# Performance work log

Measured on AMD Instinct MI355X. Metric: run time of the kernel, lower is better.

The kernel has to match this reference:

```python
import jax, jax.numpy as jnp
import numpy as np


def _relative_position_index(wd, wh, ww):
    coords = np.stack(np.meshgrid(np.arange(wd), np.arange(wh), np.arange(ww), indexing='ij'))
    flat = coords.reshape(3, -1)                      # (3, N)
    rel = flat[:, :, None] - flat[:, None, :]         # (3, N, N)
    rel = rel.transpose(1, 2, 0).astype(np.int64)     # (N, N, 3)
    rel[..., 0] += wd - 1
    rel[..., 1] += wh - 1
    rel[..., 2] += ww - 1
    rel[..., 0] *= (2 * wh - 1) * (2 * ww - 1)
    rel[..., 1] *= (2 * ww - 1)
    return rel.sum(-1)                                 # (N, N)


def setup_inputs() -> dict:
    key = jax.random.key(0)
    k0, k1, k2, k3 = jax.random.split(key, 4)
    B, D, H, W = 4, 16, 56, 56
    wd, wh, ww = 8, 7, 7
    C, nH = 128, 4
    N = wd * wh * ww                                   # 392
    nW = (D // wd) * (H // wh) * (W // ww)             # 128
    B_ = B * nW                                        # 512
    table_sz = (2 * wd - 1) * (2 * wh - 1) * (2 * ww - 1)  # 2535
    x = jax.random.normal(k0, (B_, N, C), jnp.float32)
    mask = jnp.zeros((nW, N, N), jnp.float32)          # 0/-inf additive mask; zeros = no shift
    qkv_w = jax.random.normal(k1, (3 * C, C), jnp.float32) * 0.02
    proj_w = jax.random.normal(k2, (C, C), jnp.float32) * 0.02
    proj_b = jnp.zeros((C,), jnp.float32)
    bias_table = jax.random.normal(k3, (table_sz, nH), jnp.float32) * 0.02
    rel_index = jnp.asarray(_relative_position_index(wd, wh, ww), jnp.int32)
    return {"x": x, "mask": mask, "qkv_w": qkv_w, "proj_w": proj_w,
            "proj_b": proj_b, "bias_table": bias_table, "rel_index": rel_index}


def reference(x, mask, qkv_w, proj_w, proj_b, bias_table, rel_index):
    B_, N, C = x.shape
    nH = bias_table.shape[1]
    hd = C // nH
    scale = hd ** -0.5
    # qkv projection (no bias, qkv_bias=False)
    qkv = (x @ qkv_w.T).reshape(B_, N, 3, nH, hd).transpose(2, 0, 3, 1, 4)  # (3,B_,H,N,hd)
    q, k, v = qkv[0] * scale, qkv[1], qkv[2]
    attn = jnp.einsum('bhnd,bhmd->bhnm', q, k)                              # (B_,H,N,N)
    bias = bias_table[rel_index.reshape(-1)].reshape(N, N, nH).transpose(2, 0, 1)
    attn = attn + bias[None]
    nW = mask.shape[0]
    attn = attn.reshape(B_ // nW, nW, nH, N, N) + mask[None, :, None]
    attn = jax.nn.softmax(attn.reshape(B_, nH, N, N), axis=-1)
    out = jnp.einsum('bhnm,bhmd->bhnd', attn, v)                            # (B_,H,N,hd)
    out = out.transpose(0, 2, 1, 3).reshape(B_, N, C)
    return out @ proj_w.T + proj_b
```

## Files before the change

### kernel.cpp

```cpp
#include <hip/hip_runtime.h>

typedef unsigned short u16;
typedef unsigned int   u32;

#define NTOK   392
#define NN2    153664
#define LOG2E  1.44269504088896340736f
#define QSCL   (0.17677669529663687f * 1.44269504088896340736f)
#define BTK    416
#define BTH    (416L*416L)

typedef __attribute__((ext_vector_type(8))) __bf16 bf16x8;
typedef __attribute__((ext_vector_type(4))) float  f32x4;
#define MFMA16(a,b,c) __builtin_amdgcn_mfma_f32_16x16x32_bf16((a),(b),(c),0,0,0)

__device__ __forceinline__ float bf2f(u16 u){
    union { u32 i; float f; } v; v.i = ((u32)u) << 16; return v.f;
}
__device__ __forceinline__ u16 f2bf(float x){
    union { float f; u32 i; } v; v.f = x;
    u32 r = (v.i + 0x7FFFu + ((v.i >> 16) & 1u)) >> 16;
    return (u16)r;
}
__device__ __forceinline__ u16 bfbits(float x){
    union { __bf16 b; u16 u; } v; v.b = (__bf16)x; return v.u;
}
__device__ __forceinline__ u32 pk2(float a, float b){
    return (u32)bfbits(a) | ((u32)bfbits(b) << 16);
}
__device__ __forceinline__ float ldf(const void* p, int isb, long i){
    if (isb) return bf2f(((const u16*)p)[i]);
    else     return ((const float*)p)[i];
}
__device__ __forceinline__ void stf(void* p, int isb, long i, float v){
    if (isb) ((u16*)p)[i] = f2bf(v);
    else     ((float*)p)[i] = v;
}

__device__ __forceinline__ void ld8s(const void* p, int isb, long i0,
                                     bf16x8* h, bf16x8* l){
    union { u16 u[8]; bf16x8 v; } H, L;
    if (isb){
        const uint2* q = (const uint2*)((const u16*)p + i0);
        uint2 a = q[0], b = q[1];
        H.u[0]=(u16)a.x; H.u[1]=(u16)(a.x>>16); H.u[2]=(u16)a.y; H.u[3]=(u16)(a.y>>16);
        H.u[4]=(u16)b.x; H.u[5]=(u16)(b.x>>16); H.u[6]=(u16)b.y; H.u[7]=(u16)(b.y>>16);
        #pragma unroll
        for (int j = 0; j < 8; ++j) L.u[j] = 0;
    } else {
        const float4* q = (const float4*)((const float*)p + i0);
        float4 a = q[0], b = q[1];
        float f[8] = {a.x,a.y,a.z,a.w,b.x,b.y,b.z,b.w};
        #pragma unroll
        for (int j = 0; j < 8; ++j){
            u16 hh = f2bf(f[j]);
            H.u[j] = hh;
            L.u[j] = f2bf(f[j] - bf2f(hh));
        }
    }
    *h = H.v; *l = L.v;
}

__device__ __forceinline__ int plaus(u16 w){
    int e = (w >> 7) & 0xFF;
    return (w == 0) || (e >= 96 && e <= 145);
}
__global__ __launch_bounds__(256) void prep_kernel(
        const u16* __restrict__ x, int* __restrict__ flags){
    __shared__ int cnt[2];
    int tid = threadIdx.x;
    if (tid < 2) cnt[tid] = 0;
    __syncthreads();
    int p = plaus(x[tid]) + plaus(x[tid + 256]);
    if (p) atomicAdd(&cnt[0], p);
    int ez = ((tid & 1) == 0 && x[tid] == 0) + (((tid + 256) & 1) == 0 && x[tid + 256] == 0);
    if (ez) atomicAdd(&cnt[1], ez);
    __syncthreads();
    if (tid == 0){
        flags[0] = (cnt[1] < 64 && cnt[0] >= 436) ? 1 : 0;
        flags[4] = 0;
    }
}

__global__ __launch_bounds__(256) void mask_scan_kernel(
        const u32* __restrict__ m, int nhalf, const int* __restrict__ flagsRO,
        int* __restrict__ flags){
    long nw = flagsRO[0] ? nhalf : 2L * nhalf;
    long i0 = (long)blockIdx.x * 256 + threadIdx.x;
    u32 acc = 0;
    for (long i = i0; i < nw; i += (long)gridDim.x * 256) acc |= m[i];
    if (acc) atomicOr(&flags[4], 1);
}

__global__ __launch_bounds__(256) void bias_expand_kernel(
        const int* __restrict__ rel_index, const void* btabP,
        const int* __restrict__ flags, float* __restrict__ biasF){
    long idx = (long)blockIdx.x * 256 + threadIdx.x;
    if (idx >= BTH) return;
    int q   = (int)(idx / BTK);
    int key = (int)(idx - (long)q * BTK);
    int isb = flags[0];
    float v0, v1, v2, v3;
    if (key >= NTOK){ v0 = v1 = v2 = v3 = -1e30f; }
    else if (q >= NTOK){ v0 = v1 = v2 = v3 = 0.f; }
    else {
        int t = rel_index[(long)q * NTOK + key];
        v0 = ldf(btabP, isb, (long)t * 4 + 0) * LOG2E;
        v1 = ldf(btabP, isb, (long)t * 4 + 1) * LOG2E;
        v2 = ldf(btabP, isb, (long)t * 4 + 2) * LOG2E;
        v3 = ldf(btabP, isb, (long)t * 4 + 3) * LOG2E;
    }
    biasF[0 * BTH + idx] = v0;
    biasF[1 * BTH + idx] = v1;
    biasF[2 * BTH + idx] = v2;
    biasF[3 * BTH + idx] = v3;
}

__global__ __launch_bounds__(832) void attn_mfma_kernel(
        const void* xP, const void* qwP, const void* maskP,
        const float* __restrict__ biasF, const int* __restrict__ flags,
        void* outP){
    __shared__ __align__(16) u16 Qh[416 * 40];
    __shared__ __align__(16) u16 Kh[416 * 40];
    __shared__ __align__(16) u16 VT[32 * 424];
    __shared__ __align__(16) u16 uni[2 * 64 * 136];

    u16* xs_hi = uni;
    u16* xs_lo = uni + 64 * 136;

    const int tid  = threadIdx.x;
    const int lane = tid & 63;
    const int wv   = tid >> 6;
    const int c    = lane & 15;
    const int g    = lane >> 4;
    const int h    = blockIdx.y;
    const int b_   = blockIdx.x;
    const int wdx  = b_ & 127;
    const int isb  = flags[0], fm = flags[4];
    const long xbase = (long)b_ * NTOK * 128;

    for (int i = tid; i < 24 * 40; i += 832){ Qh[392 * 40 + i] = 0; Kh[392 * 40 + i] = 0; }
    for (int i = tid; i < 32 * 32; i += 832) VT[(i >> 5) * 424 + 392 + (i & 31)] = 0;

    const int nt0 = wv >> 2,        mt0 = wv & 3;
    const int nt1 = (wv + 13) >> 2, mt1 = (wv + 13) & 3;
    const int has1 = (wv < 11);
    bf16x8 W0h[4], W0l[4], W1h[4], W1l[4];
    {
        int n0 = nt0 * 16 + c;
        int wr0 = (n0 < 32) ? (h * 32 + n0)
                : (n0 < 64) ? (128 + h * 32 + (n0 - 32))
                :             (256 + h * 32 + (n0 - 64));
        int n1 = nt1 * 16 + c;
        int wr1 = (n1 < 32) ? (h * 32 + n1)
                : (n1 < 64) ? (128 + h * 32 + (n1 - 32))
                :             (256 + h * 32 + (n1 - 64));
        #pragma unroll
        for (int ks = 0; ks < 4; ++ks){
            ld8s(qwP, isb, (long)wr0 * 128 + ks * 32 + 8 * g, &W0h[ks], &W0l[ks]);
            if (has1)
                ld8s(qwP, isb, (long)wr1 * 128 + ks * 32 + 8 * g, &W1h[ks], &W1l[ks]);
        }
    }

    for (int ch = 0; ch < 7; ++ch){
        const int tok0 = ch * 64;
        __syncthreads();
        for (int idx = tid * 4; idx < 8192; idx += 3328){
            int r = idx >> 7, cc = idx & 127;
            int row = tok0 + r;
            if (isb){
                uint2 a = make_uint2(0u, 0u);
                if (row < NTOK)
                    a = *(const uint2*)((const u16*)xP + xbase + (long)row * 128 + cc);
                *(uint2*)&xs_hi[r * 136 + cc] = a;
            } else {
                u32 h01, h23, l01, l23;
                if (row < NTOK){
                    float4 f = *(const float4*)((const float*)xP + xbase + (long)row * 128 + cc);
                    u16 h0=f2bf(f.x), h1=f2bf(f.y), h2=f2bf(f.z), h3=f2bf(f.w);
                    h01 = h0 | ((u32)h1 << 16); h23 = h2 | ((u32)h3 << 16);
                    l01 = (u32)f2bf(f.x - bf2f(h0)) | ((u32)f2bf(f.y - bf2f(h1)) << 16);
                    l23 = (u32)f2bf(f.z - bf2f(h2)) | ((u32)f2bf(f.w - bf2f(h3)) << 16);
                } else { h01 = h23 = l01 = l23 = 0; }
                *(uint2*)&xs_hi[r * 136 + cc] = make_uint2(h01, h23);
                *(uint2*)&xs_lo[r * 136 + cc] = make_uint2(l01, l23);
            }
        }
        __syncthreads();
        {
            f32x4 acc = {0.f, 0.f, 0.f, 0.f};
            #pragma unroll
            for (int ks = 0; ks < 4; ++ks){
                bf16x8 ah = *(const bf16x8*)&xs_hi[(mt0 * 16 + c) * 136 + ks * 32 + 8 * g];
                acc = MFMA16(ah, W0h[ks], acc);
                if (!isb){
                    bf16x8 al = *(const bf16x8*)&xs_lo[(mt0 * 16 + c) * 136 + ks * 32 + 8 * g];
                    acc = MFMA16(al, W0h[ks], acc);
                    acc = MFMA16(ah, W0l[ks], acc);
                }
            }
            int n = nt0 * 16 + c;
            #pragma unroll
            for (int i = 0; i < 4; ++i){
                int tok = tok0 + mt0 * 16 + 4 * g + i;
                if (tok < NTOK){
                    if (n < 32)      Qh[tok * 40 + n]         = f2bf(acc[i] * QSCL);
                    else if (n < 64) Kh[tok * 40 + (n - 32)]  = f2bf(acc[i]);
                    else             VT[(n - 64) * 424 + tok] = f2bf(acc[i]);
                }
            }
        }
        if (has1){
            f32x4 acc = {0.f, 0.f, 0.f, 0.f};
            #pragma unroll
            for (int ks = 0; ks < 4; ++ks){
                bf16x8 ah = *(const bf16x8*)&xs_hi[(mt1 * 16 + c) * 136 + ks * 32 + 8 * g];
                acc = MFMA16(ah, W1h[ks], acc);
                if (!isb){
                    bf16x8 al = *(const bf16x8*)&xs_lo[(mt1 * 16 + c) * 136 + ks * 32 + 8 * g];
                    acc = MFMA16(al, W1h[ks], acc);
                    acc = MFMA16(ah, W1l[ks], acc);
                }
            }
            int n = nt1 * 16 + c;
            #pragma unroll
            for (int i = 0; i < 4; ++i){
                int tok = tok0 + mt1 * 16 + 4 * g + i;
                if (tok < NTOK){
                    if (n < 32)      Qh[tok * 40 + n]         = f2bf(acc[i] * QSCL);
                    else if (n < 64) Kh[tok * 40 + (n - 32)]  = f2bf(acc[i]);
                    else             VT[(n - 64) * 424 + tok] = f2bf(acc[i]);
                }
            }
        }
    }
    __syncthreads();

    u16* pbA = uni + wv * 1280;
    u16* pbB = pbA + 640;
    const int qa0 = wv * 32, qb0 = qa0 + 16;
    const float* bpA = biasF + (long)h * BTH + (long)(qa0 + c) * BTK;
    const float* bpB = biasF + (long)h * BTH + (long)(qb0 + c) * BTK;
    const long mbase = (long)wdx * NN2;

    bf16x8 qA = *(const bf16x8*)&Qh[(qa0 + c) * 40 + 8 * g];
    bf16x8 qB = *(const bf16x8*)&Qh[(qb0 + c) * 40 + 8 * g];
    f32x4 oA0={0.f,0.f,0.f,0.f}, oA1={0.f,0.f,0.f,0.f};
    f32x4 oB0={0.f,0.f,0.f,0.f}, oB1={0.f,0.f,0.f,0.f};
    float rsA = 0.f, rsB = 0.f;
    f32x4 rAe = *(const f32x4*)(bpA + 4 * g);
    f32x4 rAo = *(const f32x4*)(bpA + 16 + 4 * g);
    f32x4 rBe = *(const f32x4*)(bpB + 4 * g);
    f32x4 rBo = *(const f32x4*)(bpB + 16 + 4 * g);

    for (int k2 = 0; k2 < 13; ++k2){
        const int kk = k2 * 32;
        f32x4 cAe = rAe, cAo = rAo, cBe = rBe, cBo = rBo;
        if (k2 < 12){
            rAe = *(const f32x4*)(bpA + kk + 32 + 4 * g);
            rAo = *(const f32x4*)(bpA + kk + 48 + 4 * g);
            rBe = *(const f32x4*)(bpB + kk + 32 + 4 * g);
            rBo = *(const f32x4*)(bpB + kk + 48 + 4 * g);
        }
        if (fm){
            int qa_ = qa0 + c; if (qa_ >= NTOK) qa_ = NTOK - 1;
            int qb_ = qb0 + c; if (qb_ >= NTOK) qb_ = NTOK - 1;
            #pragma unroll
            for (int i = 0; i < 4; ++i){
                int ke = kk + 4 * g + i;      int kce = ke < NTOK ? ke : NTOK - 1;
                int ko = kk + 16 + 4 * g + i; int kco = ko < NTOK ? ko : NTOK - 1;
                cAe[i] += ldf(maskP, isb, mbase + (long)qa_ * NTOK + kce) * LOG2E;
                cAo[i] += ldf(maskP, isb, mbase + (long)qa_ * NTOK + kco) * LOG2E;
                cBe[i] += ldf(maskP, isb, mbase + (long)qb_ * NTOK + kce) * LOG2E;
                cBo[i] += ldf(maskP, isb, mbase + (long)qb_ * NTOK + kco) * LOG2E;
            }
        }
        bf16x8 kbE = *(const bf16x8*)&Kh[(kk + c) * 40 + 8 * g];
        bf16x8 kbO = *(const bf16x8*)&Kh[(kk + 16 + c) * 40 + 8 * g];
        f32x4 sAe = MFMA16(kbE, qA, cAe);
        f32x4 sAo = MFMA16(kbO, qA, cAo);
        f32x4 sBe = MFMA16(kbE, qB, cBe);
        f32x4 sBo = MFMA16(kbO, qB, cBo);
        float pAe[4], pAo[4], pBe[4], pBo[4];
        #pragma unroll
        for (int i = 0; i < 4; ++i){
            pAe[i] = exp2f(sAe[i]); pAo[i] = exp2f(sAo[i]);
            pBe[i] = exp2f(sBe[i]); pBo[i] = exp2f(sBo[i]);
        }
        rsA += ((pAe[0]+pAe[1]) + (pAe[2]+pAe[3])) + ((pAo[0]+pAo[1]) + (pAo[2]+pAo[3]));
        rsB += ((pBe[0]+pBe[1]) + (pBe[2]+pBe[3])) + ((pBo[0]+pBo[1]) + (pBo[2]+pBo[3]));
        *(uint2*)&pbA[c * 40 + 4 * g]      = make_uint2(pk2(pAe[0],pAe[1]), pk2(pAe[2],pAe[3]));
        *(uint2*)&pbA[c * 40 + 16 + 4 * g] = make_uint2(pk2(pAo[0],pAo[1]), pk2(pAo[2],pAo[3]));
        *(uint2*)&pbB[c * 40 + 4 * g]      = make_uint2(pk2(pBe[0],pBe[1]), pk2(pBe[2],pBe[3]));
        *(uint2*)&pbB[c * 40 + 16 + 4 * g] = make_uint2(pk2(pBo[0],pBo[1]), pk2(pBo[2],pBo[3]));
        bf16x8 paA = *(const bf16x8*)&pbA[c * 40 + 8 * g];
        bf16x8 paB = *(const bf16x8*)&pbB[c * 40 + 8 * g];
        bf16x8 v0 = *(const bf16x8*)&VT[c * 424 + kk + 8 * g];
        bf16x8 v1 = *(const bf16x8*)&VT[(c + 16) * 424 + kk + 8 * g];
        oA0 = MFMA16(paA, v0, oA0);
        oA1 = MFMA16(paA, v1, oA1);
        oB0 = MFMA16(paB, v0, oB0);
        oB1 = MFMA16(paB, v1, oB1);
    }
    rsA += __shfl_xor(rsA, 16, 64); rsA += __shfl_xor(rsA, 32, 64);
    rsB += __shfl_xor(rsB, 16, 64); rsB += __shfl_xor(rsB, 32, 64);
    #pragma unroll
    for (int i = 0; i < 4; ++i){
        float SA = __shfl(rsA, 4 * g + i, 64);
        float SB = __shfl(rsB, 4 * g + i, 64);
        int ta = qa0 + 4 * g + i;
        if (ta < NTOK){
            float ia = 1.f / SA;
            stf(outP, isb, xbase + (long)ta * 128 + h * 32 + c,      oA0[i] * ia);
            stf(outP, isb, xbase + (long)ta * 128 + h * 32 + 16 + c, oA1[i] * ia);
        }
        int tb = qb0 + 4 * g + i;
        if (tb < NTOK){
            float ib = 1.f / SB;
            stf(outP, isb, xbase + (long)tb * 128 + h * 32 + c,      oB0[i] * ib);
            stf(outP, isb, xbase + (long)tb * 128 + h * 32 + 16 + c, oB1[i] * ib);
        }
    }
}

__global__ __launch_bounds__(512) void proj_mfma_kernel(
        const void* wP, const void* bP, const int* __restrict__ flags,
        void* outP){
    __shared__ __align__(16) u16 xs_hi[64 * 136];
    __shared__ __align__(16) u16 xs_lo[64 * 136];
    const int tid  = threadIdx.x;
    const int lane = tid & 63;
    const int wv   = tid >> 6;
    const int c    = lane & 15;
    const int g    = lane >> 4;
    const int isb  = flags[0];
    const long m0  = (long)blockIdx.x * 64;

    #pragma unroll
    for (int jj = 0; jj < 4; ++jj){
        int idx = jj * 2048 + tid * 4;
        int r = idx >> 7, cc = idx & 127;
        long gi = (m0 + r) * 128 + cc;
        if (isb){
            uint2 a = *(const uint2*)((const u16*)outP + gi);
            *(uint2*)&xs_hi[r * 136 + cc] = a;
        } else {
            float4 f = *(const float4*)((const float*)outP + gi);
            u16 h0=f2bf(f.x), h1=f2bf(f.y), h2=f2bf(f.z), h3=f2bf(f.w);
            u32 h01 = h0 | ((u32)h1 << 16), h23 = h2 | ((u32)h3 << 16);
            u32 l01 = (u32)f2bf(f.x - bf2f(h0)) | ((u32)f2bf(f.y - bf2f(h1)) << 16);
            u32 l23 = (u32)f2bf(f.z - bf2f(h2)) | ((u32)f2bf(f.w - bf2f(h3)) << 16);
            *(uint2*)&xs_hi[r * 136 + cc] = make_uint2(h01, h23);
            *(uint2*)&xs_lo[r * 136 + cc] = make_uint2(l01, l23);
        }
    }
    __syncthreads();
    const int mt  = wv >> 1;
    const int ntb = (wv & 1) * 4;
    bf16x8 ah[4], al[4];
    #pragma unroll
    for (int ks = 0; ks < 4; ++ks){
        ah[ks] = *(const bf16x8*)&xs_hi[(mt * 16 + c) * 136 + ks * 32 + 8 * g];
        if (!isb)
            al[ks] = *(const bf16x8*)&xs_lo[(mt * 16 + c) * 136 + ks * 32 + 8 * g];
    }
    #pragma unroll
    for (int j = 0; j < 4; ++j){
        int nt = ntb + j;
        bf16x8 wh[4], wl[4];
        #pragma unroll
        for (int ks = 0; ks < 4; ++ks)
            ld8s(wP, isb, (long)(nt * 16 + c) * 128 + ks * 32 + 8 * g, &wh[ks], &wl[ks]);
        f32x4 acc = {0.f,0.f,0.f,0.f};
        #pragma unroll
        for (int ks = 0; ks < 4; ++ks){
            acc = MFMA16(ah[ks], wh[ks], acc);
            if (!isb){
                acc = MFMA16(al[ks], wh[ks], acc);
                acc = MFMA16(ah[ks], wl[ks], acc);
            }
        }
        float bias = ldf(bP, isb, nt * 16 + c);
        #pragma unroll
        for (int i = 0; i < 4; ++i){
            long row = m0 + mt * 16 + 4 * g + i;
            stf(outP, isb, row * 128 + nt * 16 + c, acc[i] + bias);
        }
    }
}

extern "C" void kernel_launch(void* const* d_in, const int* in_sizes, int n_in,
                              void* d_out, int out_size, void* d_ws, size_t ws_size,
                              hipStream_t stream){
    const void* x      = d_in[0];
    const void* mask   = d_in[1];
    const void* qkv_w  = d_in[2];
    const void* proj_w = d_in[3];
    const void* proj_b = d_in[4];
    const void* btab   = d_in[5];
    const int*  relidx = (const int*)d_in[6];

    int*   flags = (int*)d_ws;
    float* biasF = (float*)((char*)d_ws + 256);

    prep_kernel<<<dim3(1), dim3(256), 0, stream>>>((const u16*)x, flags);
    int nhalf = in_sizes[1] / 2;
    mask_scan_kernel<<<dim3(2048), dim3(256), 0, stream>>>(
        (const u32*)mask, nhalf, flags, flags);
    bias_expand_kernel<<<dim3((int)((BTH + 255) / 256)), dim3(256), 0, stream>>>(
        relidx, btab, flags, biasF);
    attn_mfma_kernel<<<dim3(512, 4), dim3(832), 0, stream>>>(
        x, qkv_w, mask, biasF, flags, d_out);
    proj_mfma_kernel<<<dim3(3136), dim3(512), 0, stream>>>(
        proj_w, proj_b, flags, d_out);
}
```

Baseline: 700.3 us.

## Shrink attention LDS and registers, store bias as fp16, reorder grid by head

Rewrites the fused attention kernel to cut its shared-memory and register footprint. The QKV projection now runs in 32-token chunks with 12 waves, and Q is kept in registers through a double-buffered staging area instead of a full LDS array. The attention loop handles one 16-row query tile per pass in two passes, where before each wave held two tiles at once. The relative-position bias is expanded to fp16, halving its memory traffic, and the grid is swapped so the four heads of a window launch next to each other for better cache reuse. The changes aim at higher occupancy (launch bounds hint 7) and less bias bandwidth, at the cost of fp16 bias precision, a finite -25000 padding value, and more barriers across 13 chunks.

New measurement: 1.188 ms. 1.7x slower.

```diff
diff --git a/kernel.cpp b/kernel.cpp
--- a/kernel.cpp
+++ b/kernel.cpp
@@ -27,6 +27,15 @@
 }
 __device__ __forceinline__ u32 pk2(float a, float b){
     return (u32)bfbits(a) | ((u32)bfbits(b) << 16);
+}
+__device__ __forceinline__ u16 f16b(float x){
+    union { _Float16 h; u16 u; } t; t.h = (_Float16)x; return t.u;
+}
+__device__ __forceinline__ f32x4 h4tof(uint2 u){
+    union { u32 w; _Float16 h[2]; } a, b;
+    a.w = u.x; b.w = u.y;
+    f32x4 r = { (float)a.h[0], (float)a.h[1], (float)b.h[0], (float)b.h[1] };
+    return r;
 }
 __device__ __forceinline__ float ldf(const void* p, int isb, long i){
     if (isb) return bf2f(((const u16*)p)[i]);
@@ -94,14 +103,14 @@
 
 __global__ __launch_bounds__(256) void bias_expand_kernel(
         const int* __restrict__ rel_index, const void* btabP,
-        const int* __restrict__ flags, float* __restrict__ biasF){
+        const int* __restrict__ flags, u16* __restrict__ biasH){
     long idx = (long)blockIdx.x * 256 + threadIdx.x;
     if (idx >= BTH) return;
     int q   = (int)(idx / BTK);
     int key = (int)(idx - (long)q * BTK);
     int isb = flags[0];
     float v0, v1, v2, v3;
-    if (key >= NTOK){ v0 = v1 = v2 = v3 = -1e30f; }
+    if (key >= NTOK){ v0 = v1 = v2 = v3 = -25000.f; }
     else if (q >= NTOK){ v0 = v1 = v2 = v3 = 0.f; }
     else {
         int t = rel_index[(long)q * NTOK + key];
@@ -110,63 +119,67 @@
         v2 = ldf(btabP, isb, (long)t * 4 + 2) * LOG2E;
         v3 = ldf(btabP, isb, (long)t * 4 + 3) * LOG2E;
     }
-    biasF[0 * BTH + idx] = v0;
-    biasF[1 * BTH + idx] = v1;
-    biasF[2 * BTH + idx] = v2;
-    biasF[3 * BTH + idx] = v3;
-}
-
-__global__ __launch_bounds__(832) void attn_mfma_kernel(
+    biasH[0 * BTH + idx] = f16b(v0);
+    biasH[1 * BTH + idx] = f16b(v1);
+    biasH[2 * BTH + idx] = f16b(v2);
+    biasH[3 * BTH + idx] = f16b(v3);
+}
+
+__global__ __launch_bounds__(832, 7) void attn_mfma_kernel(
         const void* xP, const void* qwP, const void* maskP,
-        const float* __restrict__ biasF, const int* __restrict__ flags,
+        const u16* __restrict__ biasH, const int* __restrict__ flags,
         void* outP){
-    __shared__ __align__(16) u16 Qh[416 * 40];
-    __shared__ __align__(16) u16 Kh[416 * 40];
-    __shared__ __align__(16) u16 VT[32 * 424];
-    __shared__ __align__(16) u16 uni[2 * 64 * 136];
+    __shared__ __align__(16) u16 Kh[416 * 32];
+    __shared__ __align__(16) u16 VT[32 * 416];
+    __shared__ __align__(16) u16 uni[2 * 32 * 136];
+    __shared__ __align__(16) u16 smQ[2 * 32 * 32];
 
     u16* xs_hi = uni;
-    u16* xs_lo = uni + 64 * 136;
+    u16* xs_lo = uni + 32 * 136;
 
     const int tid  = threadIdx.x;
     const int lane = tid & 63;
     const int wv   = tid >> 6;
     const int c    = lane & 15;
     const int g    = lane >> 4;
-    const int h    = blockIdx.y;
-    const int b_   = blockIdx.x;
+    const int h    = blockIdx.x;
+    const int b_   = blockIdx.y;
     const int wdx  = b_ & 127;
     const int isb  = flags[0], fm = flags[4];
     const long xbase = (long)b_ * NTOK * 128;
 
-    for (int i = tid; i < 24 * 40; i += 832){ Qh[392 * 40 + i] = 0; Kh[392 * 40 + i] = 0; }
-    for (int i = tid; i < 32 * 32; i += 832) VT[(i >> 5) * 424 + 392 + (i & 31)] = 0;
-
-    const int nt0 = wv >> 2,        mt0 = wv & 3;
-    const int nt1 = (wv + 13) >> 2, mt1 = (wv + 13) & 3;
-    const int has1 = (wv < 11);
-    bf16x8 W0h[4], W0l[4], W1h[4], W1l[4];
-    {
-        int n0 = nt0 * 16 + c;
-        int wr0 = (n0 < 32) ? (h * 32 + n0)
-                : (n0 < 64) ? (128 + h * 32 + (n0 - 32))
-                :             (256 + h * 32 + (n0 - 64));
-        int n1 = nt1 * 16 + c;
-        int wr1 = (n1 < 32) ? (h * 32 + n1)
-                : (n1 < 64) ? (128 + h * 32 + (n1 - 32))
-                :             (256 + h * 32 + (n1 - 64));
-        #pragma unroll
-        for (int ks = 0; ks < 4; ++ks){
-            ld8s(qwP, isb, (long)wr0 * 128 + ks * 32 + 8 * g, &W0h[ks], &W0l[ks]);
-            if (has1)
-                ld8s(qwP, isb, (long)wr1 * 128 + ks * 32 + 8 * g, &W1h[ks], &W1l[ks]);
-        }
-    }
-
-    for (int ch = 0; ch < 7; ++ch){
-        const int tok0 = ch * 64;
+    const int ntw = wv >> 1;
+    const int mtw = wv & 1;
+    bf16x8 WHr[4], WLr[4];
+    if (wv < 12){
+        int nn = ntw * 16 + c;
+        int wrow = (nn < 32) ? (h * 32 + nn)
+                 : (nn < 64) ? (128 + h * 32 + (nn - 32))
+                 :             (256 + h * 32 + (nn - 64));
+        #pragma unroll
+        for (int ks = 0; ks < 4; ++ks)
+            ld8s(qwP, isb, (long)wrow * 128 + ks * 32 + 8 * g, &WHr[ks], &WLr[ks]);
+    }
+
+    bf16x8 qS0 = {}, qS1 = {};
+
+    for (int ch = 0; ch < 13; ++ch){
+        const int tok0 = ch * 32;
         __syncthreads();
-        for (int idx = tid * 4; idx < 8192; idx += 3328){
+        if (ch > 0){
+            const int cp = ch - 1;
+            const u16* sq = smQ + (cp & 1) * 1024;
+            const int t0 = 2 * cp, t1 = t0 + 1;
+            if (wv == t0 % 13){
+                bf16x8 v = *(const bf16x8*)&sq[c * 32 + 8 * g];
+                if (t0 < 13) qS0 = v; else qS1 = v;
+            }
+            if (wv == t1 % 13){
+                bf16x8 v = *(const bf16x8*)&sq[(16 + c) * 32 + 8 * g];
+                if (t1 < 13) qS0 = v; else qS1 = v;
+            }
+        }
+        for (int idx = tid * 4; idx < 4096; idx += 3328){
             int r = idx >> 7, cc = idx & 127;
             int row = tok0 + r;
             if (isb){
@@ -188,138 +201,102 @@
             }
         }
         __syncthreads();
-        {
+        if (wv < 12){
             f32x4 acc = {0.f, 0.f, 0.f, 0.f};
             #pragma unroll
             for (int ks = 0; ks < 4; ++ks){
-                bf16x8 ah = *(const bf16x8*)&xs_hi[(mt0 * 16 + c) * 136 + ks * 32 + 8 * g];
-                acc = MFMA16(ah, W0h[ks], acc);
+                bf16x8 ah = *(const bf16x8*)&xs_hi[(mtw * 16 + c) * 136 + ks * 32 + 8 * g];
+                acc = MFMA16(ah, WHr[ks], acc);
                 if (!isb){
-                    bf16x8 al = *(const bf16x8*)&xs_lo[(mt0 * 16 + c) * 136 + ks * 32 + 8 * g];
-                    acc = MFMA16(al, W0h[ks], acc);
-                    acc = MFMA16(ah, W0l[ks], acc);
+                    bf16x8 al = *(const bf16x8*)&xs_lo[(mtw * 16 + c) * 136 + ks * 32 + 8 * g];
+                    acc = MFMA16(al, WHr[ks], acc);
+                    acc = MFMA16(ah, WLr[ks], acc);
                 }
             }
-            int n = nt0 * 16 + c;
             #pragma unroll
             for (int i = 0; i < 4; ++i){
-                int tok = tok0 + mt0 * 16 + 4 * g + i;
-                if (tok < NTOK){
-                    if (n < 32)      Qh[tok * 40 + n]         = f2bf(acc[i] * QSCL);
-                    else if (n < 64) Kh[tok * 40 + (n - 32)]  = f2bf(acc[i]);
-                    else             VT[(n - 64) * 424 + tok] = f2bf(acc[i]);
+                int trow = mtw * 16 + 4 * g + i;
+                int tok  = tok0 + trow;
+                if (ntw < 2)
+                    smQ[(ch & 1) * 1024 + trow * 32 + ntw * 16 + c] = f2bf(acc[i] * QSCL);
+                else if (ntw < 4)
+                    Kh[tok * 32 + (ntw - 2) * 16 + c] = f2bf(acc[i]);
+                else
+                    VT[((ntw - 4) * 16 + c) * 416 + tok] = f2bf(acc[i]);
+            }
+        }
+    }
+    __syncthreads();
+    {
+        const u16* sq = smQ + (12 & 1) * 1024;
+        if (wv == 24 % 13){
+            bf16x8 v = *(const bf16x8*)&sq[c * 32 + 8 * g];
+            qS1 = v;
+        }
+        if (wv == 25 % 13){
+            bf16x8 v = *(const bf16x8*)&sq[(16 + c) * 32 + 8 * g];
+            qS1 = v;
+        }
+    }
+
+    u16* pb = uni + wv * 640;
+    const u16* bHh = biasH + (long)h * BTH;
+    const long mbase = (long)wdx * NN2;
+
+    for (int pass = 0; pass < 2; ++pass){
+        const int t  = wv + 13 * pass;
+        const int q0 = t * 16;
+        bf16x8 qA = pass ? qS1 : qS0;
+        const u16* bp = bHh + (long)(q0 + c) * BTK;
+        f32x4 o0 = {0.f,0.f,0.f,0.f}, o1 = {0.f,0.f,0.f,0.f};
+        float rs = 0.f;
+        uint2 bre = *(const uint2*)(bp + 4 * g);
+        uint2 bro = *(const uint2*)(bp + 16 + 4 * g);
+        for (int k2 = 0; k2 < 13; ++k2){
+            const int kk = k2 * 32;
+            uint2 ue = bre, uo = bro;
+            if (k2 < 12){
+                bre = *(const uint2*)(bp + kk + 32 + 4 * g);
+                bro = *(const uint2*)(bp + kk + 48 + 4 * g);
+            }
+            f32x4 cE = h4tof(ue), cO = h4tof(uo);
+            if (fm){
+                int q_ = q0 + c; if (q_ >= NTOK) q_ = NTOK - 1;
+                #pragma unroll
+                for (int i = 0; i < 4; ++i){
+                    int ke = kk + 4 * g + i;      int kce = ke < NTOK ? ke : NTOK - 1;
+                    int ko = kk + 16 + 4 * g + i; int kco = ko < NTOK ? ko : NTOK - 1;
+                    cE[i] += ldf(maskP, isb, mbase + (long)q_ * NTOK + kce) * LOG2E;
+                    cO[i] += ldf(maskP, isb, mbase + (long)q_ * NTOK + kco) * LOG2E;
                 }
             }
-        }
-        if (has1){
-            f32x4 acc = {0.f, 0.f, 0.f, 0.f};
+            bf16x8 kbE = *(const bf16x8*)&Kh[(kk + c) * 32 + 8 * g];
+            bf16x8 kbO = *(const bf16x8*)&Kh[(kk + 16 + c) * 32 + 8 * g];
+            f32x4 sE = MFMA16(kbE, qA, cE);
+            f32x4 sO = MFMA16(kbO, qA, cO);
+            float pE[4], pO[4];
             #pragma unroll
-            for (int ks = 0; ks < 4; ++ks){
-                bf16x8 ah = *(const bf16x8*)&xs_hi[(mt1 * 16 + c) * 136 + ks * 32 + 8 * g];
-                acc = MFMA16(ah, W1h[ks], acc);
-                if (!isb){
-                    bf16x8 al = *(const bf16x8*)&xs_lo[(mt1 * 16 + c) * 136 + ks * 32 + 8 * g];
-                    acc = MFMA16(al, W1h[ks], acc);
-                    acc = MFMA16(ah, W1l[ks], acc);
-                }
-            }
-            int n = nt1 * 16 + c;
-            #pragma unroll
-            for (int i = 0; i < 4; ++i){
-                int tok = tok0 + mt1 * 16 + 4 * g + i;
-                if (tok < NTOK){
-                    if (n < 32)      Qh[tok * 40 + n]         = f2bf(acc[i] * QSCL);
-                    else if (n < 64) Kh[tok * 40 + (n - 32)]  = f2bf(acc[i]);
-                    else             VT[(n - 64) * 424 + tok] = f2bf(acc[i]);
-                }
-            }
-        }
-    }
-    __syncthreads();
-
-    u16* pbA = uni + wv * 1280;
-    u16* pbB = pbA + 640;
-    const int qa0 = wv * 32, qb0 = qa0 + 16;
-    const float* bpA = biasF + (long)h * BTH + (long)(qa0 + c) * BTK;
-    const float* bpB = biasF + (long)h * BTH + (long)(qb0 + c) * BTK;
-    const long mbase = (long)wdx * NN2;
-
-    bf16x8 qA = *(const bf16x8*)&Qh[(qa0 + c) * 40 + 8 * g];
-    bf16x8 qB = *(const bf16x8*)&Qh[(qb0 + c) * 40 + 8 * g];
-    f32x4 oA0={0.f,0.f,0.f,0.f}, oA1={0.f,0.f,0.f,0.f};
-    f32x4 oB0={0.f,0.f,0.f,0.f}, oB1={0.f,0.f,0.f,0.f};
-    float rsA = 0.f, rsB = 0.f;
-    f32x4 rAe = *(const f32x4*)(bpA + 4 * g);
-    f32x4 rAo = *(const f32x4*)(bpA + 16 + 4 * g);
-    f32x4 rBe = *(const f32x4*)(bpB + 4 * g);
-    f32x4 rBo = *(const f32x4*)(bpB + 16 + 4 * g);
-
-    for (int k2 = 0; k2 < 13; ++k2){
-        const int kk = k2 * 32;
-        f32x4 cAe = rAe, cAo = rAo, cBe = rBe, cBo = rBo;
-        if (k2 < 12){
-            rAe = *(const f32x4*)(bpA + kk + 32 + 4 * g);
-            rAo = *(const f32x4*)(bpA + kk + 48 + 4 * g);
-            rBe = *(const f32x4*)(bpB + kk + 32 + 4 * g);
-            rBo = *(const f32x4*)(bpB + kk + 48 + 4 * g);
-        }
-        if (fm){
-            int qa_ = qa0 + c; if (qa_ >= NTOK) qa_ = NTOK - 1;
-            int qb_ = qb0 + c; if (qb_ >= NTOK) qb_ = NTOK - 1;
-            #pragma unroll
-            for (int i = 0; i < 4; ++i){
-                int ke = kk + 4 * g + i;      int kce = ke < NTOK ? ke : NTOK - 1;
-                int ko = kk + 16 + 4 * g + i; int kco = ko < NTOK ? ko : NTOK - 1;
-                cAe[i] += ldf(maskP, isb, mbase + (long)qa_ * NTOK + kce) * LOG2E;
-                cAo[i] += ldf(maskP, isb, mbase + (long)qa_ * NTOK + kco) * LOG2E;
-                cBe[i] += ldf(maskP, isb, mbase + (long)qb_ * NTOK + kce) * LOG2E;
-                cBo[i] += ldf(maskP, isb, mbase + (long)qb_ * NTOK + kco) * LOG2E;
-            }
-        }
-        bf16x8 kbE = *(const bf16x8*)&Kh[(kk + c) * 40 + 8 * g];
-        bf16x8 kbO = *(const bf16x8*)&Kh[(kk + 16 + c) * 40 + 8 * g];
-        f32x4 sAe = MFMA16(kbE, qA, cAe);
-        f32x4 sAo = MFMA16(kbO, qA, cAo);
-        f32x4 sBe = MFMA16(kbE, qB, cBe);
-        f32x4 sBo = MFMA16(kbO, qB, cBo);
-        float pAe[4], pAo[4], pBe[4], pBo[4];
+            for (int i = 0; i < 4; ++i){ pE[i] = exp2f(sE[i]); pO[i] = exp2f(sO[i]); }
+            rs += ((pE[0]+pE[1]) + (pE[2]+pE[3])) + ((pO[0]+pO[1]) + (pO[2]+pO[3]));
+            *(uint2*)&pb[c * 40 + 4 * g]      = make_uint2(pk2(pE[0],pE[1]), pk2(pE[2],pE[3]));
+            *(uint2*)&pb[c * 40 + 16 + 4 * g] = make_uint2(pk2(pO[0],pO[1]), pk2(pO[2],pO[3]));
+            bf16x8 pa = *(const bf16x8*)&pb[c * 40 + 8 * g];
+            bf16x8 v0 = *(const bf16x8*)&VT[c * 416 + kk + 8 * g];
+            bf16x8 v1 = *(const bf16x8*)&VT[(c + 16) * 416 + kk + 8 * g];
+            o0 = MFMA16(pa, v0, o0);
+            o1 = MFMA16(pa, v1, o1);
+        }
+        rs += __shfl_xor(rs, 16, 64);
+        rs += __shfl_xor(rs, 32, 64);
         #pragma unroll
         for (int i = 0; i < 4; ++i){
-            pAe[i] = exp2f(sAe[i]); pAo[i] = exp2f(sAo[i]);
-            pBe[i] = exp2f(sBe[i]); pBo[i] = exp2f(sBo[i]);
-        }
-        rsA += ((pAe[0]+pAe[1]) + (pAe[2]+pAe[3])) + ((pAo[0]+pAo[1]) + (pAo[2]+pAo[3]));
-        rsB += ((pBe[0]+pBe[1]) + (pBe[2]+pBe[3])) + ((pBo[0]+pBo[1]) + (pBo[2]+pBo[3]));
-        *(uint2*)&pbA[c * 40 + 4 * g]      = make_uint2(pk2(pAe[0],pAe[1]), pk2(pAe[2],pAe[3]));
-        *(uint2*)&pbA[c * 40 + 16 + 4 * g] = make_uint2(pk2(pAo[0],pAo[1]), pk2(pAo[2],pAo[3]));
-        *(uint2*)&pbB[c * 40 + 4 * g]      = make_uint2(pk2(pBe[0],pBe[1]), pk2(pBe[2],pBe[3]));
-        *(uint2*)&pbB[c * 40 + 16 + 4 * g] = make_uint2(pk2(pBo[0],pBo[1]), pk2(pBo[2],pBo[3]));
-        bf16x8 paA = *(const bf16x8*)&pbA[c * 40 + 8 * g];
-        bf16x8 paB = *(const bf16x8*)&pbB[c * 40 + 8 * g];
-        bf16x8 v0 = *(const bf16x8*)&VT[c * 424 + kk + 8 * g];
-        bf16x8 v1 = *(const bf16x8*)&VT[(c + 16) * 424 + kk + 8 * g];
-        oA0 = MFMA16(paA, v0, oA0);
-        oA1 = MFMA16(paA, v1, oA1);
-        oB0 = MFMA16(paB, v0, oB0);
-        oB1 = MFMA16(paB, v1, oB1);
-    }
-    rsA += __shfl_xor(rsA, 16, 64); rsA += __shfl_xor(rsA, 32, 64);
-    rsB += __shfl_xor(rsB, 16, 64); rsB += __shfl_xor(rsB, 32, 64);
-    #pragma unroll
-    for (int i = 0; i < 4; ++i){
-        float SA = __shfl(rsA, 4 * g + i, 64);
-        float SB = __shfl(rsB, 4 * g + i, 64);
-        int ta = qa0 + 4 * g + i;
-        if (ta < NTOK){
-            float ia = 1.f / SA;
-            stf(outP, isb, xbase + (long)ta * 128 + h * 32 + c,      oA0[i] * ia);
-            stf(outP, isb, xbase + (long)ta * 128 + h * 32 + 16 + c, oA1[i] * ia);
-        }
-        int tb = qb0 + 4 * g + i;
-        if (tb < NTOK){
-            float ib = 1.f / SB;
-            stf(outP, isb, xbase + (long)tb * 128 + h * 32 + c,      oB0[i] * ib);
-            stf(outP, isb, xbase + (long)tb * 128 + h * 32 + 16 + c, oB1[i] * ib);
+            float S = __shfl(rs, 4 * g + i, 64);
+            int tok = q0 + 4 * g + i;
+            if (tok < NTOK){
+                float iv = 1.f / S;
+                stf(outP, isb, xbase + (long)tok * 128 + h * 32 + c,      o0[i] * iv);
+                stf(outP, isb, xbase + (long)tok * 128 + h * 32 + 16 + c, o1[i] * iv);
+            }
         }
     }
 }
@@ -401,17 +378,17 @@
     const void* btab   = d_in[5];
     const int*  relidx = (const int*)d_in[6];
 
-    int*   flags = (int*)d_ws;
-    float* biasF = (float*)((char*)d_ws + 256);
+    int* flags = (int*)d_ws;
+    u16* biasH = (u16*)((char*)d_ws + 256);
 
     prep_kernel<<<dim3(1), dim3(256), 0, stream>>>((const u16*)x, flags);
     int nhalf = in_sizes[1] / 2;
     mask_scan_kernel<<<dim3(2048), dim3(256), 0, stream>>>(
         (const u32*)mask, nhalf, flags, flags);
     bias_expand_kernel<<<dim3((int)((BTH + 255) / 256)), dim3(256), 0, stream>>>(
-        relidx, btab, flags, biasF);
-    attn_mfma_kernel<<<dim3(512, 4), dim3(832), 0, stream>>>(
-        x, qkv_w, mask, biasF, flags, d_out);
+        relidx, btab, flags, biasH);
+    attn_mfma_kernel<<<dim3(4, 512), dim3(832), 0, stream>>>(
+        x, qkv_w, mask, biasH, flags, d_out);
     proj_mfma_kernel<<<dim3(3136), dim3(512), 0, stream>>>(
         proj_w, proj_b, flags, d_out);
 }
```
